# Kernel tuning notes

Hardware: AMD Instinct MI355X
Metric: run time of the kernel (lower is better)

## Reference

```python
import jax, jax.numpy as jnp
import numpy as np

B, S, D = 2, 4096, 512
H = 8
HD = D // H


def setup_inputs() -> dict:
    key = jax.random.key(0)
    k1, k2, k3, k4, k5 = jax.random.split(key, 5)
    sd = 1.0 / np.sqrt(D)
    return {
        "x": jax.random.normal(k1, (B, S, D), dtype=jnp.float32),
        "Wqkv": jax.random.normal(k2, (3 * D, D), dtype=jnp.float32) * sd,
        "bqkv": jax.random.normal(k3, (3 * D,), dtype=jnp.float32) * 0.02,
        "Wo": jax.random.normal(k4, (D, D), dtype=jnp.float32) * sd,
        "bo": jax.random.normal(k5, (D,), dtype=jnp.float32) * 0.02,
    }


def reference(x, Wqkv, bqkv, Wo, bo):
    b, s, d = x.shape
    h, hd = H, d // H
    # QKV projection (torch Linear: x @ W^T + b)
    qkv = x @ Wqkv.T + bqkv                      # [b, s, 3d]
    q, k, v = jnp.split(qkv, 3, axis=-1)         # each [b, s, d]
    # [b, s, h, hd] -> [b, h, s, hd]
    q = q.reshape(b, s, h, hd).transpose(0, 2, 1, 3)
    k = k.reshape(b, s, h, hd).transpose(0, 2, 1, 3)
    v = v.reshape(b, s, h, hd).transpose(0, 2, 1, 3)
    # causal additive mask: triu(ones, diag=1) * -1e10
    mask = jnp.triu(jnp.ones((s, s), dtype=x.dtype), k=1) * jnp.asarray(-1e10, x.dtype)
    wts = jnp.einsum("bhqd,bhkd->bhqk", q, k) / np.sqrt(hd).astype(np.float32)
    wts = wts + mask[None, None, :, :]
    wts = jax.nn.softmax(wts, axis=-1)
    y = jnp.einsum("bhqk,bhkd->bhqd", wts, v)    # [b, h, s, hd]
    y = y.transpose(0, 2, 1, 3).reshape(b, s, d) # [b, s, d]
    out = y @ Wo.T + bo
    return out
```

## Files before the change

kernel.cpp:

```cpp
#include <hip/hip_runtime.h>


typedef __bf16 bf16x8 __attribute__((ext_vector_type(8)));
typedef float f32x4 __attribute__((ext_vector_type(4)));
typedef unsigned short u16;

#define MFMA(a, b, c) __builtin_amdgcn_mfma_f32_16x16x32_bf16(a, b, c, 0, 0, 0)
#define QSCALE 0.18033688011112042f

__device__ __forceinline__ float exp2_fast(float x) {
    return __builtin_amdgcn_exp2f(x);
}
__device__ __forceinline__ u16 f2bf(float f) {
    union { __bf16 h; u16 u; } v; v.h = (__bf16)f; return v.u;
}
__device__ __forceinline__ ushort4 f4_to_bf4(float4 v) {
    ushort4 r;
    r.x = f2bf(v.x); r.y = f2bf(v.y); r.z = f2bf(v.z); r.w = f2bf(v.w);
    return r;
}
__device__ __forceinline__ void load_lds16(const u16* g, u16* l) {
    __builtin_amdgcn_global_load_lds(
        (const __attribute__((address_space(1))) void*)g,
        (__attribute__((address_space(3))) void*)l, 16, 0, 0);
}

__global__ __launch_bounds__(256) void cvt_all(
    const float* __restrict__ x, const float* __restrict__ wq,
    const float* __restrict__ wo,
    u16* __restrict__ xb, u16* __restrict__ wqb, u16* __restrict__ wob)
{
    int i = blockIdx.x * 256 + threadIdx.x;
    if (i < 1048576) {
        ((ushort4*)xb)[i] = f4_to_bf4(((const float4*)x)[i]);
    } else if (i < 1048576 + 196608) {
        int j = i - 1048576;
        ((ushort4*)wqb)[j] = f4_to_bf4(((const float4*)wq)[j]);
    } else {
        int j = i - 1048576 - 196608;
        ((ushort4*)wob)[j] = f4_to_bf4(((const float4*)wo)[j]);
    }
}

__global__ __launch_bounds__(256) void gemm_qkv_bf(
    const u16* __restrict__ X, const u16* __restrict__ W,
    const float* __restrict__ bias,
    u16* __restrict__ QY, u16* __restrict__ Kf, u16* __restrict__ Vf)
{
    __shared__ u16 As[2 * 128 * 32];
    __shared__ u16 Bs[2 * 128 * 32];
    const int K = 512;
    const int tid = threadIdx.x, wave = tid >> 6, lane = tid & 63;
    const int l15 = lane & 15, quad = lane >> 4;
    const int bm = blockIdx.x * 128, bn = blockIdx.y * 128;
    const int wr = wave >> 1, wc = wave & 1;
    const int arow = lane >> 2;
    const int acol = (lane & 3) * 8;

    f32x4 acc[4][4] = {};
#pragma unroll
    for (int ii = 0; ii < 2; ii++) {
        const int inst = wave * 2 + ii;
        const int row = inst * 16 + arow;
        load_lds16(&X[(bm + row) * K + acol], &As[inst * 512]);
        load_lds16(&W[(bn + row) * K + acol], &Bs[inst * 512]);
    }
    int cur = 0;
    for (int k0 = 0; k0 < K; k0 += 32) {
        __builtin_amdgcn_s_barrier();
        if (k0 + 32 < K) {
            const int nb = (cur ^ 1) * 4096;
#pragma unroll
            for (int ii = 0; ii < 2; ii++) {
                const int inst = wave * 2 + ii;
                const int row = inst * 16 + arow;
                load_lds16(&X[(bm + row) * K + k0 + 32 + acol], &As[nb + inst * 512]);
                load_lds16(&W[(bn + row) * K + k0 + 32 + acol], &Bs[nb + inst * 512]);
            }
            asm volatile("s_waitcnt vmcnt(4)" ::: "memory");
        } else {
            asm volatile("s_waitcnt vmcnt(0)" ::: "memory");
        }
        __builtin_amdgcn_s_barrier();
        const int cb = cur * 4096;
        bf16x8 a[4], b[4];
#pragma unroll
        for (int i = 0; i < 4; i++)
            a[i] = *(const bf16x8*)&As[cb + (wr * 64 + i * 16 + l15) * 32 + quad * 8];
#pragma unroll
        for (int j = 0; j < 4; j++)
            b[j] = *(const bf16x8*)&Bs[cb + (wc * 64 + j * 16 + l15) * 32 + quad * 8];
#pragma unroll
        for (int i = 0; i < 4; i++)
#pragma unroll
            for (int j = 0; j < 4; j++)
                acc[i][j] = MFMA(b[i], a[j], acc[i][j]);
        cur ^= 1;
    }

    const int nbase = bn + wc * 64;
    const int which = nbase >> 9;
#pragma unroll
    for (int i = 0; i < 4; i++) {
        const int d0 = nbase + i * 16 + quad * 4;
        const float4 bv = *(const float4*)&bias[d0];
        const int d0m = d0 & 511;
        const int h = d0m >> 6, hd0 = d0m & 63;
#pragma unroll
        for (int j = 0; j < 4; j++) {
            const int s_g = bm + wr * 64 + j * 16 + l15;
            const int b_ = s_g >> 12, s0 = s_g & 4095;
            const int bhh = b_ * 8 + h;
            const int kt = s0 >> 6;
            if (which == 2) {
                const int kk = s0 & 63;
                const int halfv = kk >> 5, qv = (kk >> 3) & 3, e = kk & 7;
                const int n = hd0 >> 4;
                const int lv0 = hd0 & 15;
                const size_t tb = ((size_t)(bhh * 64 + kt)) * 4096 +
                                  n * 1024 + halfv * 512 + qv * 128 + e;
#pragma unroll
                for (int r = 0; r < 4; r++) {
                    const float bvr = (r == 0) ? bv.x : (r == 1) ? bv.y : (r == 2) ? bv.z : bv.w;
                    Vf[tb + (lv0 + r) * 8] = f2bf(acc[i][j][r] + bvr);
                }
            } else if (which == 1) {
                const int jj = (s0 >> 4) & 3, lr = s0 & 15;
                const int half = hd0 >> 5, q4 = (hd0 >> 3) & 3, e0 = hd0 & 7;
                ushort4 pk;
                pk.x = f2bf(acc[i][j][0] + bv.x);
                pk.y = f2bf(acc[i][j][1] + bv.y);
                pk.z = f2bf(acc[i][j][2] + bv.z);
                pk.w = f2bf(acc[i][j][3] + bv.w);
                const size_t off = ((size_t)(bhh * 64 + kt)) * 4096 +
                                   jj * 1024 + half * 512 + q4 * 128 + lr * 8 + e0;
                *(ushort4*)&Kf[off] = pk;
            } else {
                ushort4 pk;
                pk.x = f2bf((acc[i][j][0] + bv.x) * QSCALE);
                pk.y = f2bf((acc[i][j][1] + bv.y) * QSCALE);
                pk.z = f2bf((acc[i][j][2] + bv.z) * QSCALE);
                pk.w = f2bf((acc[i][j][3] + bv.w) * QSCALE);
                *(ushort4*)&QY[((b_ * 4096 + s0) * 8 + h) * 64 + hd0] = pk;
            }
        }
    }
}

#define LS 72

__global__ __launch_bounds__(64, 2) void attn_k(
    const u16* __restrict__ QY, const u16* __restrict__ Kf, const u16* __restrict__ Vf,
    u16* __restrict__ PO, float* __restrict__ ML)
{
    __shared__ u16 Ps[16 * LS];

    const int lane = threadIdx.x;
    const int l15 = lane & 15, quad = lane >> 4;
    const int bh = blockIdx.x;
    const int b_ = bh >> 3, h = bh & 7;
    const int y = (int)blockIdx.y;
    const int p = y >> 1;
    const int seg = y & 1;

    bf16x8 ones;
#pragma unroll
    for (int i = 0; i < 8; i++) ones[i] = (__bf16)1.0f;

    const u16* KfB = &Kf[((size_t)bh * 64) * 4096 + lane * 8];
    const u16* VfB = &Vf[((size_t)bh * 64) * 4096 + lane * 8];
    u16* P = Ps;

#define LOADKV(DK, DV, KT) do {                                              \
    const u16* kp_ = KfB + (KT) * 4096;                                      \
    const u16* vp_ = VfB + (KT) * 4096;                                      \
    _Pragma("unroll")                                                        \
    for (int j_ = 0; j_ < 4; j_++) {                                         \
        DK[j_][0] = *(const bf16x8*)&kp_[j_ * 1024];                         \
        DK[j_][1] = *(const bf16x8*)&kp_[j_ * 1024 + 512];                   \
        DV[j_][0] = *(const bf16x8*)&vp_[j_ * 1024];                         \
        DV[j_][1] = *(const bf16x8*)&vp_[j_ * 1024 + 512];                   \
    }                                                                        \
} while (0)

#define TILEBODY(KC, VC, KT) do {                                            \
    const int k0_ = (KT) * 64;                                               \
    const bool nmA_ = (k0_ + 63 > base_r);                                   \
    const bool nmB_ = (k0_ + 63 > base_r + 16);                              \
    f32x4 sa_[4], sb_[4];                                                    \
    _Pragma("unroll")                                                        \
    for (int j_ = 0; j_ < 4; j_++) {                                         \
        f32x4 ia_ = {}, ib_ = {};                                            \
        if (nmA_) {                                                          \
            _Pragma("unroll")                                                \
            for (int r_ = 0; r_ < 4; r_++) {                                 \
                const int key_ = k0_ + j_ * 16 + quad * 4 + r_;              \
                ia_[r_] = (key_ > rowA) ? -1e30f : 0.0f;                     \
            }                                                                \
        }                                                                    \
        if (nmB_) {                                                          \
            _Pragma("unroll")                                                \
            for (int r_ = 0; r_ < 4; r_++) {                                 \
                const int key_ = k0_ + j_ * 16 + quad * 4 + r_;              \
                ib_[r_] = (key_ > rowA + 16) ? -1e30f : 0.0f;                \
            }                                                                \
        }                                                                    \
        ia_ = MFMA(KC[j_][0], qa0, ia_);                                     \
        sa_[j_] = MFMA(KC[j_][1], qa1, ia_);                                 \
        ib_ = MFMA(KC[j_][0], qb0, ib_);                                     \
        sb_[j_] = MFMA(KC[j_][1], qb1, ib_);                                 \
    }                                                                        \
    _Pragma("unroll")                                                        \
    for (int j_ = 0; j_ < 4; j_++) {                                         \
        ushort4 w_;                                                          \
        w_.x = f2bf(exp2_fast(sa_[j_][0]));                                  \
        w_.y = f2bf(exp2_fast(sa_[j_][1]));                                  \
        w_.z = f2bf(exp2_fast(sa_[j_][2]));                                  \
        w_.w = f2bf(exp2_fast(sa_[j_][3]));                                  \
        *(ushort4*)&P[l15 * LS + j_ * 16 + quad * 4] = w_;                   \
    }                                                                        \
    float spb_[4][4];                                                        \
    _Pragma("unroll")                                                        \
    for (int j_ = 0; j_ < 4; j_++)                                           \
        _Pragma("unroll")                                                    \
        for (int r_ = 0; r_ < 4; r_++)                                       \
            spb_[j_][r_] = exp2_fast(sb_[j_][r_]);                           \
    bf16x8 pfa0_ = *(const bf16x8*)&P[l15 * LS + quad * 8];                  \
    bf16x8 pfa1_ = *(const bf16x8*)&P[l15 * LS + 32 + quad * 8];             \
    _Pragma("unroll")                                                        \
    for (int j_ = 0; j_ < 4; j_++) {                                         \
        ushort4 w_;                                                          \
        w_.x = f2bf(spb_[j_][0]); w_.y = f2bf(spb_[j_][1]);                  \
        w_.z = f2bf(spb_[j_][2]); w_.w = f2bf(spb_[j_][3]);                  \
        *(ushort4*)&P[l15 * LS + j_ * 16 + quad * 4] = w_;                   \
    }                                                                        \
    lacc_a = MFMA(ones, pfa0_, lacc_a);                                      \
    lacc_a = MFMA(ones, pfa1_, lacc_a);                                      \
    _Pragma("unroll")                                                        \
    for (int n_ = 0; n_ < 4; n_++) {                                         \
        oa[n_] = MFMA(VC[n_][0], pfa0_, oa[n_]);                             \
        oa[n_] = MFMA(VC[n_][1], pfa1_, oa[n_]);                             \
    }                                                                        \
    bf16x8 pfb0_ = *(const bf16x8*)&P[l15 * LS + quad * 8];                  \
    bf16x8 pfb1_ = *(const bf16x8*)&P[l15 * LS + 32 + quad * 8];             \
    lacc_b = MFMA(ones, pfb0_, lacc_b);                                      \
    lacc_b = MFMA(ones, pfb1_, lacc_b);                                      \
    _Pragma("unroll")                                                        \
    for (int n_ = 0; n_ < 4; n_++) {                                         \
        ob[n_] = MFMA(VC[n_][0], pfb0_, ob[n_]);                             \
        ob[n_] = MFMA(VC[n_][1], pfb1_, ob[n_]);                             \
    }                                                                        \
} while (0)

    for (int phase = 0; phase < 2; phase++) {
        const int qt32 = phase ? (127 - p) : p;
        const int nt = (qt32 >> 1) + 1;
        const int hlf = (nt + 1) >> 1;
        const int t0 = seg ? hlf : 0;
        const int t1 = seg ? nt : hlf;
        const int base_r = qt32 * 32;

        const u16* qpa = &QY[((b_ * 4096 + base_r + l15) * 8 + h) * 64];
        const u16* qpb = qpa + 16 * 8 * 64;
        bf16x8 qa0 = *(const bf16x8*)&qpa[quad * 8];
        bf16x8 qa1 = *(const bf16x8*)&qpa[32 + quad * 8];
        bf16x8 qb0 = *(const bf16x8*)&qpb[quad * 8];
        bf16x8 qb1 = *(const bf16x8*)&qpb[32 + quad * 8];

        f32x4 oa[4] = {}, ob[4] = {};
        f32x4 lacc_a = {}, lacc_b = {};
        const int rowA = base_r + l15;

        bf16x8 kR[4][2], vR[4][2], kS[4][2], vS[4][2];
        if (t0 < t1) LOADKV(kR, vR, t0);
        for (int kt = t0; kt < t1; kt += 2) {
            const bool has1 = (kt + 1 < t1);
            if (has1) LOADKV(kS, vS, kt + 1);
            TILEBODY(kR, vR, kt);
            if (has1) {
                if (kt + 2 < t1) LOADKV(kR, vR, kt + 2);
                TILEBODY(kS, vS, kt + 1);
            }
        }

        u16* ppa = &PO[(size_t)seg * 4194304 +
                       (size_t)((b_ * 4096 + base_r + l15) * 8 + h) * 64];
        u16* ppb = ppa + 16 * 8 * 64;
#pragma unroll
        for (int n = 0; n < 4; n++) {
            ushort4 wa;
            wa.x = f2bf(oa[n][0]);
            wa.y = f2bf(oa[n][1]);
            wa.z = f2bf(oa[n][2]);
            wa.w = f2bf(oa[n][3]);
            *(ushort4*)&ppa[n * 16 + quad * 4] = wa;
            ushort4 wb;
            wb.x = f2bf(ob[n][0]);
            wb.y = f2bf(ob[n][1]);
            wb.z = f2bf(ob[n][2]);
            wb.w = f2bf(ob[n][3]);
            *(ushort4*)&ppb[n * 16 + quad * 4] = wb;
        }
        if (quad == 0) {
            ML[(seg * 16 + bh) * 4096 + base_r + l15] = lacc_a[0];
            ML[(seg * 16 + bh) * 4096 + base_r + 16 + l15] = lacc_b[0];
        }
    }
#undef LOADKV
#undef TILEBODY
}

__global__ __launch_bounds__(256) void merge_k(
    const u16* __restrict__ PO, const float* __restrict__ ML, u16* __restrict__ Y)
{
    const int flat = blockIdx.x * 256 + threadIdx.x;
    const int rs = flat >> 6;
    const int rem = flat & 63;
    const int h = rem >> 3, c = rem & 7;
    const int b_ = rs >> 12, s = rs & 4095;
    const int bh = b_ * 8 + h;
    const float l0 = ML[bh * 4096 + s];
    const float l1 = ML[(16 + bh) * 4096 + s];
    const float inv = 1.0f / (l0 + l1);

    const size_t base = (size_t)(rs * 8 + h) * 64 + c * 8;
    bf16x8 x0 = *(const bf16x8*)&PO[base];
    bf16x8 x1 = *(const bf16x8*)&PO[4194304 + base];
    ushort4 lo, hi;
    lo.x = f2bf(((float)x0[0] + (float)x1[0]) * inv);
    lo.y = f2bf(((float)x0[1] + (float)x1[1]) * inv);
    lo.z = f2bf(((float)x0[2] + (float)x1[2]) * inv);
    lo.w = f2bf(((float)x0[3] + (float)x1[3]) * inv);
    hi.x = f2bf(((float)x0[4] + (float)x1[4]) * inv);
    hi.y = f2bf(((float)x0[5] + (float)x1[5]) * inv);
    hi.z = f2bf(((float)x0[6] + (float)x1[6]) * inv);
    hi.w = f2bf(((float)x0[7] + (float)x1[7]) * inv);
    *(ushort4*)&Y[base] = lo;
    *(ushort4*)&Y[base + 4] = hi;
}

__global__ __launch_bounds__(256) void gemm_o_bf(
    const u16* __restrict__ X, const u16* __restrict__ W,
    const float* __restrict__ bias, float* __restrict__ Out)
{
    __shared__ u16 As[2 * 128 * 32];
    __shared__ u16 Bs[2 * 128 * 32];
    const int K = 512;
    const int tid = threadIdx.x, wave = tid >> 6, lane = tid & 63;
    const int l15 = lane & 15, quad = lane >> 4;
    const int bm = blockIdx.x * 128, bn = blockIdx.y * 128;
    const int wr = wave >> 1, wc = wave & 1;
    const int arow = lane >> 2;
    const int acol = (lane & 3) * 8;

    f32x4 acc[4][4] = {};
#pragma unroll
    for (int ii = 0; ii < 2; ii++) {
        const int inst = wave * 2 + ii;
        const int row = inst * 16 + arow;
        load_lds16(&X[(bm + row) * K + acol], &As[inst * 512]);
        load_lds16(&W[(bn + row) * K + acol], &Bs[inst * 512]);
    }
    int cur = 0;
    for (int k0 = 0; k0 < K; k0 += 32) {
        __builtin_amdgcn_s_barrier();
        if (k0 + 32 < K) {
            const int nb = (cur ^ 1) * 4096;
#pragma unroll
            for (int ii = 0; ii < 2; ii++) {
                const int inst = wave * 2 + ii;
                const int row = inst * 16 + arow;
                load_lds16(&X[(bm + row) * K + k0 + 32 + acol], &As[nb + inst * 512]);
                load_lds16(&W[(bn + row) * K + k0 + 32 + acol], &Bs[nb + inst * 512]);
            }
            asm volatile("s_waitcnt vmcnt(4)" ::: "memory");
        } else {
            asm volatile("s_waitcnt vmcnt(0)" ::: "memory");
        }
        __builtin_amdgcn_s_barrier();
        const int cb = cur * 4096;
        bf16x8 a[4], b[4];
#pragma unroll
        for (int i = 0; i < 4; i++)
            a[i] = *(const bf16x8*)&As[cb + (wr * 64 + i * 16 + l15) * 32 + quad * 8];
#pragma unroll
        for (int j = 0; j < 4; j++)
            b[j] = *(const bf16x8*)&Bs[cb + (wc * 64 + j * 16 + l15) * 32 + quad * 8];
#pragma unroll
        for (int i = 0; i < 4; i++)
#pragma unroll
            for (int j = 0; j < 4; j++)
                acc[i][j] = MFMA(b[i], a[j], acc[i][j]);
        cur ^= 1;
    }
#pragma unroll
    for (int i = 0; i < 4; i++) {
        const int n0 = bn + wc * 64 + i * 16 + quad * 4;
        const float4 bv = *(const float4*)&bias[n0];
#pragma unroll
        for (int j = 0; j < 4; j++) {
            const int m = bm + wr * 64 + j * 16 + l15;
            float4 ov;
            ov.x = acc[i][j][0] + bv.x;
            ov.y = acc[i][j][1] + bv.y;
            ov.z = acc[i][j][2] + bv.z;
            ov.w = acc[i][j][3] + bv.w;
            *(float4*)&Out[(size_t)m * 512 + n0] = ov;
        }
    }
}

extern "C" void kernel_launch(void* const* d_in, const int* in_sizes, int n_in,
                              void* d_out, int out_size, void* d_ws, size_t ws_size,
                              hipStream_t stream) {
    (void)in_sizes; (void)n_in; (void)out_size; (void)ws_size;
    const float* x    = (const float*)d_in[0];
    const float* Wqkv = (const float*)d_in[1];
    const float* bqkv = (const float*)d_in[2];
    const float* Wo   = (const float*)d_in[3];
    const float* bo   = (const float*)d_in[4];
    float* out = (float*)d_out;

    u16* qy_ws = (u16*)d_ws;
    u16* kf_ws = qy_ws + 4194304;
    u16* vf_ws = kf_ws + 4194304;
    float* ml  = (float*)(vf_ws + 4194304);
    u16* wqkvb = (u16*)(ml + 262144);
    u16* wob   = wqkvb + 786432;
    u16* xb    = (u16*)d_out;
    u16* po    = (u16*)d_out;

    cvt_all<<<5120, 256, 0, stream>>>(x, Wqkv, Wo, xb, wqkvb, wob);
    gemm_qkv_bf<<<dim3(64, 12), 256, 0, stream>>>(xb, wqkvb, bqkv, qy_ws, kf_ws, vf_ws);
    attn_k<<<dim3(16, 128), 64, 0, stream>>>(qy_ws, kf_ws, vf_ws, po, ml);
    merge_k<<<2048, 256, 0, stream>>>(po, ml, qy_ws);
    gemm_o_bf<<<dim3(64, 4), 256, 0, stream>>>(qy_ws, wob, bo, out);
}
```

Measured before the change: 172.8 us.

## Split K/V loads with inline-asm global loads and explicit vmcnt waits in attention

The attention kernel's combined K+V double-buffer prefetch is split into separate K and V loads, issued as inline-asm global_load_dwordx4 with immediate offsets. Each tile body is split into a QK/softmax half and a PV half, gated by hand-placed s_waitcnt vmcnt counts. The V buffer drops from two copies to one, which cuts vector register pressure, and PV can overlap the still-pending loads. The risk is that the compiler cannot see the asynchronous load semantics, so correctness depends on the manual wait counts matching the outstanding loads.

```diff
diff --git a/kernel.cpp b/kernel.cpp
--- a/kernel.cpp
+++ b/kernel.cpp
@@ -149,6 +149,15 @@
 
 #define LS 72
 
+#define GLD(dst, base, OFF)                                                  \
+    asm volatile("global_load_dwordx4 %0, %1, off offset:" #OFF              \
+                 : "=v"(dst) : "v"(base))
+
+#define WAITV(N) do {                                                        \
+    asm volatile("s_waitcnt vmcnt(" #N ")" ::: "memory");                    \
+    __builtin_amdgcn_sched_barrier(0);                                       \
+} while (0)
+
 __global__ __launch_bounds__(64, 2) void attn_k(
     const u16* __restrict__ QY, const u16* __restrict__ Kf, const u16* __restrict__ Vf,
     u16* __restrict__ PO, float* __restrict__ ML)
@@ -171,19 +180,25 @@
     const u16* VfB = &Vf[((size_t)bh * 64) * 4096 + lane * 8];
     u16* P = Ps;
 
-#define LOADKV(DK, DV, KT) do {                                              \
-    const u16* kp_ = KfB + (KT) * 4096;                                      \
-    const u16* vp_ = VfB + (KT) * 4096;                                      \
-    _Pragma("unroll")                                                        \
-    for (int j_ = 0; j_ < 4; j_++) {                                         \
-        DK[j_][0] = *(const bf16x8*)&kp_[j_ * 1024];                         \
-        DK[j_][1] = *(const bf16x8*)&kp_[j_ * 1024 + 512];                   \
-        DV[j_][0] = *(const bf16x8*)&vp_[j_ * 1024];                         \
-        DV[j_][1] = *(const bf16x8*)&vp_[j_ * 1024 + 512];                   \
-    }                                                                        \
+#define LOADK(DK, KT) do {                                                   \
+    const u16* ka_ = KfB + (size_t)(KT) * 4096;                              \
+    const u16* kb_ = ka_ + 2048;                                             \
+    GLD(DK[0][0], ka_, 0);    GLD(DK[0][1], ka_, 1024);                      \
+    GLD(DK[1][0], ka_, 2048); GLD(DK[1][1], ka_, 3072);                      \
+    GLD(DK[2][0], kb_, 0);    GLD(DK[2][1], kb_, 1024);                      \
+    GLD(DK[3][0], kb_, 2048); GLD(DK[3][1], kb_, 3072);                      \
 } while (0)
 
-#define TILEBODY(KC, VC, KT) do {                                            \
+#define LOADV(DV, KT) do {                                                   \
+    const u16* va_ = VfB + (size_t)(KT) * 4096;                              \
+    const u16* vb_ = va_ + 2048;                                             \
+    GLD(DV[0][0], va_, 0);    GLD(DV[0][1], va_, 1024);                      \
+    GLD(DV[1][0], va_, 2048); GLD(DV[1][1], va_, 3072);                      \
+    GLD(DV[2][0], vb_, 0);    GLD(DV[2][1], vb_, 1024);                      \
+    GLD(DV[3][0], vb_, 2048); GLD(DV[3][1], vb_, 3072);                      \
+} while (0)
+
+#define TILE_A(KC, KT) do {                                                  \
     const int k0_ = (KT) * 64;                                               \
     const bool nmA_ = (k0_ + 63 > base_r);                                   \
     const bool nmB_ = (k0_ + 63 > base_r + 16);                              \
@@ -219,27 +234,29 @@
         w_.w = f2bf(exp2_fast(sa_[j_][3]));                                  \
         *(ushort4*)&P[l15 * LS + j_ * 16 + quad * 4] = w_;                   \
     }                                                                        \
-    float spb_[4][4];                                                        \
     _Pragma("unroll")                                                        \
     for (int j_ = 0; j_ < 4; j_++)                                           \
         _Pragma("unroll")                                                    \
         for (int r_ = 0; r_ < 4; r_++)                                       \
-            spb_[j_][r_] = exp2_fast(sb_[j_][r_]);                           \
-    bf16x8 pfa0_ = *(const bf16x8*)&P[l15 * LS + quad * 8];                  \
-    bf16x8 pfa1_ = *(const bf16x8*)&P[l15 * LS + 32 + quad * 8];             \
+            spb[j_][r_] = exp2_fast(sb_[j_][r_]);                            \
+    pfa0 = *(const bf16x8*)&P[l15 * LS + quad * 8];                          \
+    pfa1 = *(const bf16x8*)&P[l15 * LS + 32 + quad * 8];                     \
     _Pragma("unroll")                                                        \
     for (int j_ = 0; j_ < 4; j_++) {                                         \
         ushort4 w_;                                                          \
-        w_.x = f2bf(spb_[j_][0]); w_.y = f2bf(spb_[j_][1]);                  \
-        w_.z = f2bf(spb_[j_][2]); w_.w = f2bf(spb_[j_][3]);                  \
+        w_.x = f2bf(spb[j_][0]); w_.y = f2bf(spb[j_][1]);                    \
+        w_.z = f2bf(spb[j_][2]); w_.w = f2bf(spb[j_][3]);                    \
         *(ushort4*)&P[l15 * LS + j_ * 16 + quad * 4] = w_;                   \
     }                                                                        \
-    lacc_a = MFMA(ones, pfa0_, lacc_a);                                      \
-    lacc_a = MFMA(ones, pfa1_, lacc_a);                                      \
+} while (0)
+
+#define TILE_B(VC) do {                                                      \
+    lacc_a = MFMA(ones, pfa0, lacc_a);                                       \
+    lacc_a = MFMA(ones, pfa1, lacc_a);                                       \
     _Pragma("unroll")                                                        \
     for (int n_ = 0; n_ < 4; n_++) {                                         \
-        oa[n_] = MFMA(VC[n_][0], pfa0_, oa[n_]);                             \
-        oa[n_] = MFMA(VC[n_][1], pfa1_, oa[n_]);                             \
+        oa[n_] = MFMA(VC[n_][0], pfa0, oa[n_]);                              \
+        oa[n_] = MFMA(VC[n_][1], pfa1, oa[n_]);                              \
     }                                                                        \
     bf16x8 pfb0_ = *(const bf16x8*)&P[l15 * LS + quad * 8];                  \
     bf16x8 pfb1_ = *(const bf16x8*)&P[l15 * LS + 32 + quad * 8];             \
@@ -260,26 +277,39 @@
         const int t1 = seg ? nt : hlf;
         const int base_r = qt32 * 32;
 
-        const u16* qpa = &QY[((b_ * 4096 + base_r + l15) * 8 + h) * 64];
+        const u16* qpa = &QY[((b_ * 4096 + base_r + l15) * 8 + h) * 64 + quad * 8];
         const u16* qpb = qpa + 16 * 8 * 64;
-        bf16x8 qa0 = *(const bf16x8*)&qpa[quad * 8];
-        bf16x8 qa1 = *(const bf16x8*)&qpa[32 + quad * 8];
-        bf16x8 qb0 = *(const bf16x8*)&qpb[quad * 8];
-        bf16x8 qb1 = *(const bf16x8*)&qpb[32 + quad * 8];
+        bf16x8 qa0, qa1, qb0, qb1;
+        GLD(qa0, qpa, 0);
+        GLD(qa1, qpa, 64);
+        GLD(qb0, qpb, 0);
+        GLD(qb1, qpb, 64);
 
         f32x4 oa[4] = {}, ob[4] = {};
         f32x4 lacc_a = {}, lacc_b = {};
         const int rowA = base_r + l15;
 
-        bf16x8 kR[4][2], vR[4][2], kS[4][2], vS[4][2];
-        if (t0 < t1) LOADKV(kR, vR, t0);
+        float spb[4][4];
+        bf16x8 pfa0, pfa1;
+        bf16x8 kR[4][2], kS[4][2], vv[4][2];
+
+        if (t0 < t1) LOADK(kR, t0);
         for (int kt = t0; kt < t1; kt += 2) {
-            const bool has1 = (kt + 1 < t1);
-            if (has1) LOADKV(kS, vS, kt + 1);
-            TILEBODY(kR, vR, kt);
-            if (has1) {
-                if (kt + 2 < t1) LOADKV(kR, vR, kt + 2);
-                TILEBODY(kS, vS, kt + 1);
+            const bool h1 = (kt + 1 < t1);
+            LOADV(vv, kt);
+            if (h1) LOADK(kS, kt + 1);
+            if (h1) { WAITV(16); } else { WAITV(8); }
+            TILE_A(kR, kt);
+            if (h1) { WAITV(8); } else { WAITV(0); }
+            TILE_B(vv);
+            if (h1) {
+                const bool h2 = (kt + 2 < t1);
+                LOADV(vv, kt + 1);
+                if (h2) LOADK(kR, kt + 2);
+                if (h2) { WAITV(16); } else { WAITV(8); }
+                TILE_A(kS, kt + 1);
+                if (h2) { WAITV(8); } else { WAITV(0); }
+                TILE_B(vv);
             }
         }
 
@@ -306,8 +336,10 @@
             ML[(seg * 16 + bh) * 4096 + base_r + 16 + l15] = lacc_b[0];
         }
     }
-#undef LOADKV
-#undef TILEBODY
+#undef LOADK
+#undef LOADV
+#undef TILE_A
+#undef TILE_B
 }
 
 __global__ __launch_bounds__(256) void merge_k(
```

After: 166.8 us. -3.5%, faster.
